# Optimization experiments

Measured on AMD Instinct MI355X. Metric: run time of the kernel, lower is better.

Reference implementation:

```python
import jax, jax.numpy as jnp
import numpy as np

B, T, C, H, NC = 512, 256, 512, 512, 96  # batch, encoder steps, channels, hidden, num classes


def setup_inputs() -> dict:
    key = jax.random.key(0)
    ks = jax.random.split(key, 12)
    def w(k, shape, fan):
        return (jax.random.normal(k, shape, jnp.float32) / np.sqrt(fan)).astype(jnp.float32)
    labels = jax.random.randint(ks[0], (B,), 0, NC)
    return {
        "prev_h": jax.random.normal(ks[1], (B, H), jnp.float32),
        "prev_c": jax.random.normal(ks[2], (B, H), jnp.float32),
        "batch_H": jax.random.normal(ks[3], (B, T, C), jnp.float32),
        "char_onehots": jax.nn.one_hot(labels, NC, dtype=jnp.float32),
        "Wi": w(ks[4], (C, H), C),            # i2h kernel (no bias)
        "Wh": w(ks[5], (H, H), H),            # h2h kernel
        "bh": jnp.zeros((H,), jnp.float32),    # h2h bias
        "Ws": w(ks[6], (H, 1), H),            # score kernel (no bias)
        "K": w(ks[7], (C + NC, 4 * H), C + NC),  # LSTM input kernel (i,f,g,o)
        "R": w(ks[8], (H, 4 * H), H),            # LSTM recurrent kernel
        "b": jnp.zeros((4 * H,), jnp.float32),    # LSTM bias
    }


def reference(prev_h, prev_c, batch_H, char_onehots, Wi, Wh, bh, Ws, K, R, b):
    # Additive (Bahdanau) attention
    proj = jnp.einsum('btc,ch->bth', batch_H, Wi)                  # [B,T,H]
    hp = prev_h @ Wh + bh                                          # [B,H]
    e = jnp.einsum('bth,h->bt', jnp.tanh(proj + hp[:, None, :]), Ws[:, 0])  # [B,T]
    alpha = jax.nn.softmax(e, axis=1)                              # [B,T]
    context = jnp.einsum('bt,btc->bc', alpha, batch_H)             # [B,C]
    # LSTMCell step (keras gate order: i, f, g, o; sigmoid recurrent act, tanh act)
    x = jnp.concatenate([context, char_onehots], axis=1)           # [B,C+NC]
    z = x @ K + prev_h @ R + b                                     # [B,4H]
    i, f, g, o = jnp.split(z, 4, axis=1)
    c_new = jax.nn.sigmoid(f) * prev_c + jax.nn.sigmoid(i) * jnp.tanh(g)
    h_new = jax.nn.sigmoid(o) * jnp.tanh(c_new)
    return (h_new, c_new, alpha[:, :, None])  # ((h,c), alpha[B,T,1])
```

## Files before the change

kernel.cpp:

```cpp
#include <hip/hip_runtime.h>
#include <hip/hip_bf16.h>
#include <stdint.h>

#define KFULL 1120
#define N4H   2048
#define MTOT  131072

typedef float f32x4 __attribute__((ext_vector_type(4)));
typedef __bf16 bf16x8 __attribute__((ext_vector_type(8)));
typedef unsigned short u16;

__device__ __forceinline__ u16 f2bf_bits(float f){
  __bf16 b = (__bf16)f;
  union { __bf16 b; u16 u; } cv; cv.b = b;
  return cv.u;
}
__device__ __forceinline__ float sigf(float x){ return 1.f / (1.f + __expf(-x)); }
__device__ __forceinline__ float tanh_fast(float x){ return 1.f - 2.f / (__expf(2.f * x) + 1.f); }
__device__ __forceinline__ int swz(int row){ return (row ^ (row >> 2)) & 3; }

__global__ void prep_w(const float* __restrict__ Wi, const float* __restrict__ Wh,
                       const float* __restrict__ Km, const float* __restrict__ R,
                       u16* __restrict__ wiT, u16* __restrict__ whT, u16* __restrict__ wfT){
  int idx = blockIdx.x * 256 + threadIdx.x;
  if (idx < 524288){
    const float* src = (idx < 262144) ? Wi : Wh;
    u16* dst = (idx < 262144) ? wiT : whT;
    int e = idx & 262143;
    int n = e & 511, kk = (e >> 9) & 31, s = e >> 14;
    float v = src[(size_t)(s * 32 + kk) * 512 + n];
    int dkk = (kk & 7) | ((((kk >> 3) ^ swz(n)) & 3) << 3);
    dst[((size_t)s * 512 + n) * 32 + dkk] = f2bf_bits(v);
  } else {
    int e = idx - 524288;
    if (e >= 35 * 2048 * 32) return;
    int n = e & 2047, kk = (e >> 11) & 31, s = e >> 16;
    int k = s * 32 + kk;
    float v = (k < 608) ? Km[(size_t)k * 2048 + n] : R[(size_t)(k - 608) * 2048 + n];
    int dkk = (kk & 7) | ((((kk >> 3) ^ swz(n)) & 3) << 3);
    wfT[((size_t)s * 2048 + n) * 32 + dkk] = f2bf_bits(v);
  }
}

__global__ void prep_x(const float* __restrict__ onehots, const float* __restrict__ prev_h,
                       float* __restrict__ x_full){
  int idx = blockIdx.x * 256 + threadIdx.x;
  if (idx >= 512 * 608) return;
  int b = idx / 608, c = idx % 608;
  float v = (c < 96) ? onehots[b * 96 + c] : prev_h[b * 512 + (c - 96)];
  x_full[(size_t)b * KFULL + 512 + c] = v;
}

template<int EPI>
__launch_bounds__(256, 3)
__global__ void gemm128(const float* __restrict__ A, int lda, int ksteps,
                        const u16* __restrict__ Bt, int ntot,
                        float* __restrict__ outp, size_t partStride,
                        const float* __restrict__ hpart, const float* __restrict__ bh,
                        const float* __restrict__ Ws, float* __restrict__ epart){
  __shared__ u16 smA[128 * 32];
  __shared__ u16 smB[128 * 32];
  __shared__ float smHp[128];
  __shared__ float smWs[128];
  __shared__ float smRed[2][128];

  const int tid  = threadIdx.x;
  const int lane = tid & 63, w = tid >> 6;
  const int wr = w >> 1, wc = w & 1;
  const int fr = lane & 15, g = lane >> 4;

  int m0, n0, s0;
  if (EPI == 1){
    int bid = blockIdx.x;
    int sw = (bid & 7) * 512 + (bid >> 3);
    m0 = (sw >> 2) * 128;
    n0 = (sw & 3) * 128;
    s0 = 0;
  } else {
    m0 = blockIdx.x * 128;
    n0 = blockIdx.y * 128;
    s0 = blockIdx.z * ksteps;
    outp += (size_t)blockIdx.z * partStride;
  }

  if (EPI == 1 && tid < 128){
    int b = m0 >> 8;
    float h = bh[n0 + tid];
    #pragma unroll
    for (int p = 0; p < 4; ++p) h += hpart[(size_t)p * 262144 + (size_t)b * 512 + n0 + tid];
    smHp[tid] = h;
    smWs[tid] = Ws[n0 + tid];
  }

  f32x4 acc[4][4] = {};

  const int ar = tid >> 2;
  const int ac = (tid & 3) * 8;
  const float* ap = A + (size_t)(m0 + ar) * lda + ac;
  const int sz  = swz(ar);
  const int ab0 = ar * 64 + (((tid & 3) ^ sz) << 4);
  const int ab1 = ab0 + 64 * 64;

  for (int s = 0; s < ksteps; ++s){
    const int kc = (s0 + s) * 32;
    const char* bsrc = (const char*)Bt + ((size_t)(s0 + s) * ntot + n0) * 64;
    #pragma unroll
    for (int j = 0; j < 2; ++j){
      int off = w * 2048 + j * 1024;
      __builtin_amdgcn_global_load_lds(
        (const __attribute__((address_space(1))) void*)(bsrc + off + lane * 16),
        (__attribute__((address_space(3))) void*)((char*)smB + off),
        16, 0, 0);
    }
    float4 a0 = *(const float4*)(ap + kc);
    float4 a1 = *(const float4*)(ap + kc + 4);
    float4 a2 = *(const float4*)(ap + (size_t)64 * lda + kc);
    float4 a3 = *(const float4*)(ap + (size_t)64 * lda + kc + 4);
    bf16x8 w0, w1;
    w0[0]=(__bf16)a0.x; w0[1]=(__bf16)a0.y; w0[2]=(__bf16)a0.z; w0[3]=(__bf16)a0.w;
    w0[4]=(__bf16)a1.x; w0[5]=(__bf16)a1.y; w0[6]=(__bf16)a1.z; w0[7]=(__bf16)a1.w;
    w1[0]=(__bf16)a2.x; w1[1]=(__bf16)a2.y; w1[2]=(__bf16)a2.z; w1[3]=(__bf16)a2.w;
    w1[4]=(__bf16)a3.x; w1[5]=(__bf16)a3.y; w1[6]=(__bf16)a3.z; w1[7]=(__bf16)a3.w;
    *(bf16x8*)((char*)smA + ab0) = w0;
    *(bf16x8*)((char*)smA + ab1) = w1;
    __syncthreads();

    bf16x8 af[4];
    #pragma unroll
    for (int m = 0; m < 4; ++m){
      int rl = wr * 64 + m * 16 + fr;
      af[m] = *(const bf16x8*)((const char*)smA + rl * 64 + ((g ^ swz(rl)) << 4));
    }
    #pragma unroll
    for (int n = 0; n < 4; ++n){
      int nl = wc * 64 + n * 16 + fr;
      bf16x8 bfv = *(const bf16x8*)((const char*)smB + nl * 64 + ((g ^ swz(nl)) << 4));
      #pragma unroll
      for (int m = 0; m < 4; ++m)
        acc[m][n] = __builtin_amdgcn_mfma_f32_16x16x32_bf16(af[m], bfv, acc[m][n], 0, 0, 0);
    }
    __syncthreads();
  }

  if (EPI == 0){
    #pragma unroll
    for (int n = 0; n < 4; ++n){
      int col = n0 + wc * 64 + n * 16 + fr;
      #pragma unroll
      for (int m = 0; m < 4; ++m){
        int row = m0 + wr * 64 + m * 16 + g * 4;
        #pragma unroll
        for (int j = 0; j < 4; ++j)
          outp[(size_t)(row + j) * ntot + col] = acc[m][n][j];
      }
    }
  } else {
    float p[16] = {};
    #pragma unroll
    for (int n = 0; n < 4; ++n){
      int col = wc * 64 + n * 16 + fr;
      float hpv = smHp[col], wsv = smWs[col];
      #pragma unroll
      for (int m = 0; m < 4; ++m)
        #pragma unroll
        for (int j = 0; j < 4; ++j)
          p[m * 4 + j] += tanh_fast(acc[m][n][j] + hpv) * wsv;
    }
    #pragma unroll
    for (int mask = 1; mask < 16; mask <<= 1)
      #pragma unroll
      for (int i = 0; i < 16; ++i)
        p[i] += __shfl_xor(p[i], mask);
    if (fr == 0){
      #pragma unroll
      for (int m = 0; m < 4; ++m)
        #pragma unroll
        for (int j = 0; j < 4; ++j)
          smRed[wc][wr * 64 + m * 16 + g * 4 + j] = p[m * 4 + j];
    }
    __syncthreads();
    if (tid < 128){
      int nb = n0 >> 7;
      epart[(size_t)nb * MTOT + m0 + tid] = smRed[0][tid] + smRed[1][tid];
    }
  }
}

__global__ void ctx_softmax(const float* __restrict__ epart, const float* __restrict__ batch_H,
                            float* __restrict__ x_full, float* __restrict__ alpha_out){
  __shared__ float sa[256];
  __shared__ float red[4], red2[4];
  __shared__ f32x4 sred[8][32];
  int b = blockIdx.x, q = blockIdx.y, tid = threadIdx.x;

  float e = 0.f;
  #pragma unroll
  for (int p = 0; p < 4; ++p) e += epart[(size_t)p * MTOT + b * 256 + tid];
  float m = e;
  #pragma unroll
  for (int mask = 1; mask < 64; mask <<= 1) m = fmaxf(m, __shfl_xor(m, mask));
  int w = tid >> 6;
  if ((tid & 63) == 0) red[w] = m;
  __syncthreads();
  m = fmaxf(fmaxf(red[0], red[1]), fmaxf(red[2], red[3]));
  float ev = __expf(e - m);
  float s = ev;
  #pragma unroll
  for (int mask = 1; mask < 64; mask <<= 1) s += __shfl_xor(s, mask);
  if ((tid & 63) == 0) red2[w] = s;
  __syncthreads();
  s = red2[0] + red2[1] + red2[2] + red2[3];
  float a = ev / s;
  sa[tid] = a;
  if (q == 0) alpha_out[(size_t)b * 256 + tid] = a;
  __syncthreads();

  int c4 = tid & 31, tq = tid >> 5;
  const float4* bhp = (const float4*)(batch_H + (size_t)b * 131072) + (size_t)tq * 32 * 128 + q * 32 + c4;
  f32x4 acc = {0.f, 0.f, 0.f, 0.f};
  #pragma unroll 4
  for (int t = 0; t < 32; ++t){
    float av = sa[tq * 32 + t];
    float4 v = bhp[(size_t)t * 128];
    acc[0] += av * v.x; acc[1] += av * v.y; acc[2] += av * v.z; acc[3] += av * v.w;
  }
  sred[tq][c4] = acc;
  __syncthreads();
  if (tid < 32){
    f32x4 o = sred[0][tid];
    #pragma unroll
    for (int r = 1; r < 8; ++r){
      f32x4 v = sred[r][tid];
      o[0] += v[0]; o[1] += v[1]; o[2] += v[2]; o[3] += v[3];
    }
    float4 st; st.x = o[0]; st.y = o[1]; st.z = o[2]; st.w = o[3];
    *(float4*)(x_full + (size_t)b * KFULL + q * 128 + tid * 4) = st;
  }
}

__global__ void gates_k(const float* __restrict__ zpart, const float* __restrict__ bias,
                        const float* __restrict__ prev_c, float* __restrict__ out){
  int idx = blockIdx.x * 256 + threadIdx.x;
  int b = idx >> 9, h = idx & 511;
  float zi = bias[h], zf = bias[512 + h], zg = bias[1024 + h], zo = bias[1536 + h];
  #pragma unroll
  for (int p = 0; p < 5; ++p){
    const float* zr = zpart + (size_t)p * 1048576 + (size_t)b * N4H;
    zi += zr[h]; zf += zr[512 + h]; zg += zr[1024 + h]; zo += zr[1536 + h];
  }
  float c = sigf(zf) * prev_c[idx] + sigf(zi) * tanh_fast(zg);
  float hn = sigf(zo) * tanh_fast(c);
  out[idx] = hn;
  out[262144 + idx] = c;
}

extern "C" void kernel_launch(void* const* d_in, const int* in_sizes, int n_in,
                              void* d_out, int out_size, void* d_ws, size_t ws_size,
                              hipStream_t stream){
  const float* prev_h  = (const float*)d_in[0];
  const float* prev_c  = (const float*)d_in[1];
  const float* batch_H = (const float*)d_in[2];
  const float* onehots = (const float*)d_in[3];
  const float* Wi      = (const float*)d_in[4];
  const float* Wh      = (const float*)d_in[5];
  const float* bh      = (const float*)d_in[6];
  const float* Ws      = (const float*)d_in[7];
  const float* Km      = (const float*)d_in[8];
  const float* R       = (const float*)d_in[9];
  const float* bb      = (const float*)d_in[10];
  float* out = (float*)d_out;

  char* ws = (char*)d_ws;
  u16*  wiT    = (u16*)(ws + 0);
  u16*  whT    = (u16*)(ws + 524288);
  u16*  wfT    = (u16*)(ws + 1048576);
  float* hpart = (float*)(ws + 5636096);
  float* epart = (float*)(ws + 9830400);
  float* x_full= (float*)(ws + 11927552);
  float* zpart = (float*)(ws + 14221312);

  float* alpha = out + 524288;

  prep_w<<<11008, 256, 0, stream>>>(Wi, Wh, Km, R, wiT, whT, wfT);
  prep_x<<<1216, 256, 0, stream>>>(onehots, prev_h, x_full);
  gemm128<0><<<dim3(4, 4, 4), 256, 0, stream>>>(prev_h, 512, 4, whT, 512,
                                                hpart, 262144, nullptr, nullptr, nullptr, nullptr);
  gemm128<1><<<dim3(4096, 1, 1), 256, 0, stream>>>(batch_H, 512, 16, wiT, 512,
                                                   nullptr, 0, hpart, bh, Ws, epart);
  ctx_softmax<<<dim3(512, 4), 256, 0, stream>>>(epart, batch_H, x_full, alpha);
  gemm128<0><<<dim3(4, 16, 5), 256, 0, stream>>>(x_full, KFULL, 7, wfT, N4H,
                                                 zpart, 1048576, nullptr, nullptr, nullptr, nullptr);
  gates_k<<<1024, 256, 0, stream>>>(zpart, bb, prev_c, out);
}
```

Before: 205.5 us.

## Split attention GEMM into double-buffered 512-thread kernel with 128x256 tiles

Replaces the templated attention GEMM with a dedicated kernel that uses 8 waves and 128x256 output tiles, so each A tile is loaded once per half of the hidden dimension instead of once per quarter. It double-buffers A and B in LDS and prefetches the next k-step with explicit waitcnt and barriers, overlapping global loads with MFMA work. The score partials drop from four to two per row, and the softmax kernel reads only two. The change costs more LDS and registers per block, which lowers occupancy, and relies on hand-placed waitcnt ordering being correct.

```diff
diff --git a/kernel.cpp b/kernel.cpp
--- a/kernel.cpp
+++ b/kernel.cpp
@@ -51,46 +51,21 @@
   x_full[(size_t)b * KFULL + 512 + c] = v;
 }
 
-template<int EPI>
 __launch_bounds__(256, 3)
-__global__ void gemm128(const float* __restrict__ A, int lda, int ksteps,
-                        const u16* __restrict__ Bt, int ntot,
-                        float* __restrict__ outp, size_t partStride,
-                        const float* __restrict__ hpart, const float* __restrict__ bh,
-                        const float* __restrict__ Ws, float* __restrict__ epart){
+__global__ void gemm_small(const float* __restrict__ A, int lda, int ksteps,
+                           const u16* __restrict__ Bt, int ntot,
+                           float* __restrict__ outp, size_t partStride){
   __shared__ u16 smA[128 * 32];
   __shared__ u16 smB[128 * 32];
-  __shared__ float smHp[128];
-  __shared__ float smWs[128];
-  __shared__ float smRed[2][128];
 
   const int tid  = threadIdx.x;
   const int lane = tid & 63, w = tid >> 6;
   const int wr = w >> 1, wc = w & 1;
   const int fr = lane & 15, g = lane >> 4;
-
-  int m0, n0, s0;
-  if (EPI == 1){
-    int bid = blockIdx.x;
-    int sw = (bid & 7) * 512 + (bid >> 3);
-    m0 = (sw >> 2) * 128;
-    n0 = (sw & 3) * 128;
-    s0 = 0;
-  } else {
-    m0 = blockIdx.x * 128;
-    n0 = blockIdx.y * 128;
-    s0 = blockIdx.z * ksteps;
-    outp += (size_t)blockIdx.z * partStride;
-  }
-
-  if (EPI == 1 && tid < 128){
-    int b = m0 >> 8;
-    float h = bh[n0 + tid];
-    #pragma unroll
-    for (int p = 0; p < 4; ++p) h += hpart[(size_t)p * 262144 + (size_t)b * 512 + n0 + tid];
-    smHp[tid] = h;
-    smWs[tid] = Ws[n0 + tid];
-  }
+  const int m0 = blockIdx.x * 128;
+  const int n0 = blockIdx.y * 128;
+  const int s0 = blockIdx.z * ksteps;
+  outp += (size_t)blockIdx.z * partStride;
 
   f32x4 acc[4][4] = {};
 
@@ -142,48 +117,154 @@
     __syncthreads();
   }
 
-  if (EPI == 0){
-    #pragma unroll
-    for (int n = 0; n < 4; ++n){
-      int col = n0 + wc * 64 + n * 16 + fr;
+  #pragma unroll
+  for (int n = 0; n < 4; ++n){
+    int col = n0 + wc * 64 + n * 16 + fr;
+    #pragma unroll
+    for (int m = 0; m < 4; ++m){
+      int row = m0 + wr * 64 + m * 16 + g * 4;
       #pragma unroll
-      for (int m = 0; m < 4; ++m){
-        int row = m0 + wr * 64 + m * 16 + g * 4;
-        #pragma unroll
-        for (int j = 0; j < 4; ++j)
-          outp[(size_t)(row + j) * ntot + col] = acc[m][n][j];
-      }
-    }
-  } else {
-    float p[16] = {};
-    #pragma unroll
-    for (int n = 0; n < 4; ++n){
-      int col = wc * 64 + n * 16 + fr;
-      float hpv = smHp[col], wsv = smWs[col];
+      for (int j = 0; j < 4; ++j)
+        outp[(size_t)(row + j) * ntot + col] = acc[m][n][j];
+    }
+  }
+}
+
+__launch_bounds__(512, 2)
+__global__ void gemm_attn(const float* __restrict__ A,
+                          const u16* __restrict__ Bt,
+                          const float* __restrict__ hpart,
+                          const float* __restrict__ bh,
+                          const float* __restrict__ Wsv,
+                          float* __restrict__ epart){
+  __shared__ u16 smA[2][128 * 32];
+  __shared__ u16 smB[2][256 * 32];
+  __shared__ float smHp[256];
+  __shared__ float smWs[256];
+  __shared__ float smRed[4][128];
+
+  const int tid  = threadIdx.x;
+  const int lane = tid & 63, w = tid >> 6;
+  const int wr = w >> 2, wc = w & 3;
+  const int fr = lane & 15, g = lane >> 4;
+  const int m0 = blockIdx.x * 128;
+  const int nb = blockIdx.y;
+  const int n0 = nb * 256;
+  const int b  = blockIdx.x >> 1;
+
+  if (tid < 256){
+    float h = bh[n0 + tid];
+    #pragma unroll
+    for (int p = 0; p < 4; ++p) h += hpart[(size_t)p * 262144 + (size_t)b * 512 + n0 + tid];
+    smHp[tid] = h;
+    smWs[tid] = Wsv[n0 + tid];
+  }
+  asm volatile("s_waitcnt vmcnt(0) lgkmcnt(0)" ::: "memory");
+
+  f32x4 acc[4][4] = {};
+
+  const int arow = tid >> 2;
+  const int achk = tid & 3;
+  const float* aglob = A + (size_t)(m0 + arow) * 512 + achk * 8;
+  const int awoff = arow * 64 + ((achk ^ swz(arow)) << 4);
+
+  float4 pa0, pa1;
+
+#define ISSUE_B(sabs, c) do {                                              \
+    const char* bsrc = (const char*)Bt + ((size_t)(sabs) * 512 + n0) * 64; \
+    _Pragma("unroll")                                                      \
+    for (int j = 0; j < 2; ++j){                                           \
+      int off = j * 8192 + w * 1024;                                       \
+      __builtin_amdgcn_global_load_lds(                                    \
+        (const __attribute__((address_space(1))) void*)(bsrc + off + lane * 16), \
+        (__attribute__((address_space(3))) void*)((char*)&smB[c][0] + off),\
+        16, 0, 0);                                                         \
+    }                                                                      \
+  } while(0)
+
+#define LOAD_A(sabs) do {                                                  \
+    pa0 = *(const float4*)(aglob + (size_t)(sabs) * 32);                   \
+    pa1 = *(const float4*)(aglob + (size_t)(sabs) * 32 + 4);               \
+  } while(0)
+
+#define WRITE_A(c) do {                                                    \
+    bf16x8 v;                                                              \
+    v[0]=(__bf16)pa0.x; v[1]=(__bf16)pa0.y; v[2]=(__bf16)pa0.z; v[3]=(__bf16)pa0.w; \
+    v[4]=(__bf16)pa1.x; v[5]=(__bf16)pa1.y; v[6]=(__bf16)pa1.z; v[7]=(__bf16)pa1.w; \
+    *(bf16x8*)((char*)&smA[c][0] + awoff) = v;                             \
+  } while(0)
+
+#define COMPUTE(c) do {                                                    \
+    bf16x8 af[4];                                                          \
+    _Pragma("unroll")                                                      \
+    for (int m = 0; m < 4; ++m){                                           \
+      int rl = wr * 64 + m * 16 + fr;                                      \
+      af[m] = *(const bf16x8*)((const char*)&smA[c][0] + rl * 64 + ((g ^ swz(rl)) << 4)); \
+    }                                                                      \
+    _Pragma("unroll")                                                      \
+    for (int n = 0; n < 4; ++n){                                           \
+      int nl = wc * 64 + n * 16 + fr;                                      \
+      bf16x8 bfv = *(const bf16x8*)((const char*)&smB[c][0] + nl * 64 + ((g ^ swz(nl)) << 4)); \
+      _Pragma("unroll")                                                    \
+      for (int m = 0; m < 4; ++m)                                          \
+        acc[m][n] = __builtin_amdgcn_mfma_f32_16x16x32_bf16(af[m], bfv, acc[m][n], 0, 0, 0); \
+    }                                                                      \
+  } while(0)
+
+  LOAD_A(0);
+  ISSUE_B(0, 0);
+  asm volatile("" ::: "memory");
+  WRITE_A(0);
+  LOAD_A(1);
+
+  for (int s = 0; s < 16; ++s){
+    if (s < 15) asm volatile("s_waitcnt vmcnt(2)" ::: "memory");
+    else        asm volatile("s_waitcnt vmcnt(0)" ::: "memory");
+    asm volatile("s_waitcnt lgkmcnt(0)" ::: "memory");
+    __builtin_amdgcn_s_barrier();
+    asm volatile("" ::: "memory");
+    COMPUTE(s & 1);
+    if (s < 15){
+      ISSUE_B(s + 1, (s + 1) & 1);
+      asm volatile("" ::: "memory");
+      WRITE_A((s + 1) & 1);
+      if (s < 14) LOAD_A(s + 2);
+    }
+  }
+
+#undef ISSUE_B
+#undef LOAD_A
+#undef WRITE_A
+#undef COMPUTE
+
+  float p[16] = {};
+  #pragma unroll
+  for (int n = 0; n < 4; ++n){
+    int col = wc * 64 + n * 16 + fr;
+    float hpv = smHp[col], wsv = smWs[col];
+    #pragma unroll
+    for (int m = 0; m < 4; ++m)
       #pragma unroll
-      for (int m = 0; m < 4; ++m)
-        #pragma unroll
-        for (int j = 0; j < 4; ++j)
-          p[m * 4 + j] += tanh_fast(acc[m][n][j] + hpv) * wsv;
-    }
-    #pragma unroll
-    for (int mask = 1; mask < 16; mask <<= 1)
+      for (int j = 0; j < 4; ++j)
+        p[m * 4 + j] += tanh_fast(acc[m][n][j] + hpv) * wsv;
+  }
+  #pragma unroll
+  for (int mask = 1; mask < 16; mask <<= 1)
+    #pragma unroll
+    for (int i = 0; i < 16; ++i)
+      p[i] += __shfl_xor(p[i], mask);
+  __syncthreads();
+  if (fr == 0){
+    #pragma unroll
+    for (int m = 0; m < 4; ++m)
       #pragma unroll
-      for (int i = 0; i < 16; ++i)
-        p[i] += __shfl_xor(p[i], mask);
-    if (fr == 0){
-      #pragma unroll
-      for (int m = 0; m < 4; ++m)
-        #pragma unroll
-        for (int j = 0; j < 4; ++j)
-          smRed[wc][wr * 64 + m * 16 + g * 4 + j] = p[m * 4 + j];
-    }
-    __syncthreads();
-    if (tid < 128){
-      int nb = n0 >> 7;
-      epart[(size_t)nb * MTOT + m0 + tid] = smRed[0][tid] + smRed[1][tid];
-    }
-  }
+      for (int j = 0; j < 4; ++j)
+        smRed[wc][wr * 64 + m * 16 + g * 4 + j] = p[m * 4 + j];
+  }
+  __syncthreads();
+  if (tid < 128)
+    epart[(size_t)nb * MTOT + m0 + tid] =
+      smRed[0][tid] + smRed[1][tid] + smRed[2][tid] + smRed[3][tid];
 }
 
 __global__ void ctx_softmax(const float* __restrict__ epart, const float* __restrict__ batch_H,
@@ -193,9 +274,7 @@
   __shared__ f32x4 sred[8][32];
   int b = blockIdx.x, q = blockIdx.y, tid = threadIdx.x;
 
-  float e = 0.f;
-  #pragma unroll
-  for (int p = 0; p < 4; ++p) e += epart[(size_t)p * MTOT + b * 256 + tid];
+  float e = epart[(size_t)b * 256 + tid] + epart[MTOT + (size_t)b * 256 + tid];
   float m = e;
   #pragma unroll
   for (int mask = 1; mask < 64; mask <<= 1) m = fmaxf(m, __shfl_xor(m, mask));
@@ -283,12 +362,11 @@
 
   prep_w<<<11008, 256, 0, stream>>>(Wi, Wh, Km, R, wiT, whT, wfT);
   prep_x<<<1216, 256, 0, stream>>>(onehots, prev_h, x_full);
-  gemm128<0><<<dim3(4, 4, 4), 256, 0, stream>>>(prev_h, 512, 4, whT, 512,
-                                                hpart, 262144, nullptr, nullptr, nullptr, nullptr);
-  gemm128<1><<<dim3(4096, 1, 1), 256, 0, stream>>>(batch_H, 512, 16, wiT, 512,
-                                                   nullptr, 0, hpart, bh, Ws, epart);
+  gemm_small<<<dim3(4, 4, 4), 256, 0, stream>>>(prev_h, 512, 4, whT, 512,
+                                                hpart, 262144);
+  gemm_attn<<<dim3(1024, 2), 512, 0, stream>>>(batch_H, wiT, hpart, bh, Ws, epart);
   ctx_softmax<<<dim3(512, 4), 256, 0, stream>>>(epart, batch_H, x_full, alpha);
-  gemm128<0><<<dim3(4, 16, 5), 256, 0, stream>>>(x_full, KFULL, 7, wfT, N4H,
-                                                 zpart, 1048576, nullptr, nullptr, nullptr, nullptr);
+  gemm_small<<<dim3(4, 16, 5), 256, 0, stream>>>(x_full, KFULL, 7, wfT, N4H,
+                                                 zpart, 1048576);
   gates_k<<<1024, 256, 0, stream>>>(zpart, bb, prev_c, out);
 }
```

After: 209.2 us. About the same (+1.8%).

## Restructure attention GEMM: whole-K A tile in LDS, B fragments from global

Applied to the files above, without the earlier changes.

The fused attention-score GEMM now uses 64x256 tiles: each block loads its full 64-row A slab (all 16 K-steps) into LDS once as bf16 and streams Wi fragments straight from global into registers with double buffering, dropping the per-step syncthreads. Wi is stored unswizzled so per-lane global reads are contiguous. The N split shrinks from 4 to 2 partials, so softmax sums two partials. This removes per-K-step barriers and LDS staging for B, at the cost of 64KB LDS per block, more registers and lower occupancy (launch bounds 2).

```diff
diff --git a/kernel.cpp b/kernel.cpp
--- a/kernel.cpp
+++ b/kernel.cpp
@@ -29,7 +29,8 @@
     int e = idx & 262143;
     int n = e & 511, kk = (e >> 9) & 31, s = e >> 14;
     float v = src[(size_t)(s * 32 + kk) * 512 + n];
-    int dkk = (kk & 7) | ((((kk >> 3) ^ swz(n)) & 3) << 3);
+    int dkk = (idx < 262144) ? kk
+            : ((kk & 7) | ((((kk >> 3) ^ swz(n)) & 3) << 3));
     dst[((size_t)s * 512 + n) * 32 + dkk] = f2bf_bits(v);
   } else {
     int e = idx - 524288;
@@ -51,46 +52,21 @@
   x_full[(size_t)b * KFULL + 512 + c] = v;
 }
 
-template<int EPI>
 __launch_bounds__(256, 3)
-__global__ void gemm128(const float* __restrict__ A, int lda, int ksteps,
-                        const u16* __restrict__ Bt, int ntot,
-                        float* __restrict__ outp, size_t partStride,
-                        const float* __restrict__ hpart, const float* __restrict__ bh,
-                        const float* __restrict__ Ws, float* __restrict__ epart){
+__global__ void gemm_small(const float* __restrict__ A, int lda, int ksteps,
+                           const u16* __restrict__ Bt, int ntot,
+                           float* __restrict__ outp, size_t partStride){
   __shared__ u16 smA[128 * 32];
   __shared__ u16 smB[128 * 32];
-  __shared__ float smHp[128];
-  __shared__ float smWs[128];
-  __shared__ float smRed[2][128];
 
   const int tid  = threadIdx.x;
   const int lane = tid & 63, w = tid >> 6;
   const int wr = w >> 1, wc = w & 1;
   const int fr = lane & 15, g = lane >> 4;
-
-  int m0, n0, s0;
-  if (EPI == 1){
-    int bid = blockIdx.x;
-    int sw = (bid & 7) * 512 + (bid >> 3);
-    m0 = (sw >> 2) * 128;
-    n0 = (sw & 3) * 128;
-    s0 = 0;
-  } else {
-    m0 = blockIdx.x * 128;
-    n0 = blockIdx.y * 128;
-    s0 = blockIdx.z * ksteps;
-    outp += (size_t)blockIdx.z * partStride;
-  }
-
-  if (EPI == 1 && tid < 128){
-    int b = m0 >> 8;
-    float h = bh[n0 + tid];
-    #pragma unroll
-    for (int p = 0; p < 4; ++p) h += hpart[(size_t)p * 262144 + (size_t)b * 512 + n0 + tid];
-    smHp[tid] = h;
-    smWs[tid] = Ws[n0 + tid];
-  }
+  const int m0 = blockIdx.x * 128;
+  const int n0 = blockIdx.y * 128;
+  const int s0 = blockIdx.z * ksteps;
+  outp += (size_t)blockIdx.z * partStride;
 
   f32x4 acc[4][4] = {};
 
@@ -142,48 +118,133 @@
     __syncthreads();
   }
 
-  if (EPI == 0){
+  #pragma unroll
+  for (int n = 0; n < 4; ++n){
+    int col = n0 + wc * 64 + n * 16 + fr;
+    #pragma unroll
+    for (int m = 0; m < 4; ++m){
+      int row = m0 + wr * 64 + m * 16 + g * 4;
+      #pragma unroll
+      for (int j = 0; j < 4; ++j)
+        outp[(size_t)(row + j) * ntot + col] = acc[m][n][j];
+    }
+  }
+}
+
+__launch_bounds__(256, 2)
+__global__ void gemm_attn(const float* __restrict__ A,
+                          const u16* __restrict__ Bt,
+                          const float* __restrict__ hpart,
+                          const float* __restrict__ bh,
+                          const float* __restrict__ Wsv,
+                          float* __restrict__ epart){
+  __shared__ u16 smA[16][64 * 32];
+
+  const int tid  = threadIdx.x;
+  const int lane = tid & 63, w = tid >> 6;
+  const int fr = lane & 15, g = lane >> 4;
+  const int bid = blockIdx.x;
+  const int m0 = (bid >> 1) * 64;
+  const int nb = bid & 1;
+  const int n0 = nb * 256;
+  const int b  = m0 >> 8;
+
+  const int arow = tid >> 2;
+  const float* ag = A + (size_t)(m0 + arow) * 512 + (tid & 3) * 8;
+  const int awbase = arow * 64 + (((tid & 3) ^ swz(arow)) << 4);
+  float4 av[32];
+  #pragma unroll
+  for (int s = 0; s < 16; ++s){
+    av[2 * s]     = *(const float4*)(ag + s * 32);
+    av[2 * s + 1] = *(const float4*)(ag + s * 32 + 4);
+  }
+  #pragma unroll
+  for (int s = 0; s < 16; ++s){
+    bf16x8 v;
+    v[0]=(__bf16)av[2*s].x;   v[1]=(__bf16)av[2*s].y;
+    v[2]=(__bf16)av[2*s].z;   v[3]=(__bf16)av[2*s].w;
+    v[4]=(__bf16)av[2*s+1].x; v[5]=(__bf16)av[2*s+1].y;
+    v[6]=(__bf16)av[2*s+1].z; v[7]=(__bf16)av[2*s+1].w;
+    *(bf16x8*)((char*)&smA[s][0] + awbase) = v;
+  }
+
+  float hpv[4], wsv[4];
+  #pragma unroll
+  for (int n = 0; n < 4; ++n){
+    int col = n0 + w * 64 + n * 16 + fr;
+    float h = bh[col];
+    #pragma unroll
+    for (int p = 0; p < 4; ++p) h += hpart[(size_t)p * 262144 + (size_t)b * 512 + col];
+    hpv[n] = h;
+    wsv[n] = Wsv[col];
+  }
+
+  __syncthreads();
+
+  const u16* bbase = Bt + ((size_t)(n0 + w * 64 + fr)) * 32 + g * 8;
+  bf16x8 bA[4], bB[4];
+  #pragma unroll
+  for (int nf = 0; nf < 4; ++nf)
+    bA[nf] = *(const bf16x8*)(bbase + (size_t)nf * 16 * 32);
+
+  f32x4 acc[4][4] = {};
+
+  #pragma unroll
+  for (int s = 0; s < 16; ++s){
+    if (s + 1 < 16){
+      if ((s & 1) == 0){
+        #pragma unroll
+        for (int nf = 0; nf < 4; ++nf)
+          bB[nf] = *(const bf16x8*)(bbase + ((size_t)(s + 1) * 512 + nf * 16) * 32);
+      } else {
+        #pragma unroll
+        for (int nf = 0; nf < 4; ++nf)
+          bA[nf] = *(const bf16x8*)(bbase + ((size_t)(s + 1) * 512 + nf * 16) * 32);
+      }
+    }
+    bf16x8 af[4];
+    #pragma unroll
+    for (int m = 0; m < 4; ++m){
+      int rl = m * 16 + fr;
+      af[m] = *(const bf16x8*)((const char*)&smA[s][0] + rl * 64 + ((g ^ swz(rl)) << 4));
+    }
     #pragma unroll
     for (int n = 0; n < 4; ++n){
-      int col = n0 + wc * 64 + n * 16 + fr;
-      #pragma unroll
-      for (int m = 0; m < 4; ++m){
-        int row = m0 + wr * 64 + m * 16 + g * 4;
-        #pragma unroll
-        for (int j = 0; j < 4; ++j)
-          outp[(size_t)(row + j) * ntot + col] = acc[m][n][j];
-      }
-    }
-  } else {
-    float p[16] = {};
-    #pragma unroll
-    for (int n = 0; n < 4; ++n){
-      int col = wc * 64 + n * 16 + fr;
-      float hpv = smHp[col], wsv = smWs[col];
+      bf16x8 bfv = ((s & 1) == 0) ? bA[n] : bB[n];
       #pragma unroll
       for (int m = 0; m < 4; ++m)
-        #pragma unroll
-        for (int j = 0; j < 4; ++j)
-          p[m * 4 + j] += tanh_fast(acc[m][n][j] + hpv) * wsv;
-    }
-    #pragma unroll
-    for (int mask = 1; mask < 16; mask <<= 1)
-      #pragma unroll
-      for (int i = 0; i < 16; ++i)
-        p[i] += __shfl_xor(p[i], mask);
-    if (fr == 0){
-      #pragma unroll
-      for (int m = 0; m < 4; ++m)
-        #pragma unroll
-        for (int j = 0; j < 4; ++j)
-          smRed[wc][wr * 64 + m * 16 + g * 4 + j] = p[m * 4 + j];
-    }
-    __syncthreads();
-    if (tid < 128){
-      int nb = n0 >> 7;
-      epart[(size_t)nb * MTOT + m0 + tid] = smRed[0][tid] + smRed[1][tid];
-    }
-  }
+        acc[m][n] = __builtin_amdgcn_mfma_f32_16x16x32_bf16(af[m], bfv, acc[m][n], 0, 0, 0);
+    }
+  }
+
+  float p[16] = {};
+  #pragma unroll
+  for (int n = 0; n < 4; ++n){
+    #pragma unroll
+    for (int m = 0; m < 4; ++m)
+      #pragma unroll
+      for (int j = 0; j < 4; ++j)
+        p[m * 4 + j] += tanh_fast(acc[m][n][j] + hpv[n]) * wsv[n];
+  }
+  #pragma unroll
+  for (int mask = 1; mask < 16; mask <<= 1)
+    #pragma unroll
+    for (int i = 0; i < 16; ++i)
+      p[i] += __shfl_xor(p[i], mask);
+
+  float* smRed = (float*)&smA[0][0];
+  __syncthreads();
+  if (fr == 0){
+    #pragma unroll
+    for (int m = 0; m < 4; ++m)
+      #pragma unroll
+      for (int j = 0; j < 4; ++j)
+        smRed[w * 64 + m * 16 + g * 4 + j] = p[m * 4 + j];
+  }
+  __syncthreads();
+  if (tid < 64)
+    epart[(size_t)nb * MTOT + m0 + tid] =
+      smRed[tid] + smRed[64 + tid] + smRed[128 + tid] + smRed[192 + tid];
 }
 
 __global__ void ctx_softmax(const float* __restrict__ epart, const float* __restrict__ batch_H,
@@ -193,9 +254,7 @@
   __shared__ f32x4 sred[8][32];
   int b = blockIdx.x, q = blockIdx.y, tid = threadIdx.x;
 
-  float e = 0.f;
-  #pragma unroll
-  for (int p = 0; p < 4; ++p) e += epart[(size_t)p * MTOT + b * 256 + tid];
+  float e = epart[(size_t)b * 256 + tid] + epart[MTOT + (size_t)b * 256 + tid];
   float m = e;
   #pragma unroll
   for (int mask = 1; mask < 64; mask <<= 1) m = fmaxf(m, __shfl_xor(m, mask));
@@ -283,12 +342,11 @@
 
   prep_w<<<11008, 256, 0, stream>>>(Wi, Wh, Km, R, wiT, whT, wfT);
   prep_x<<<1216, 256, 0, stream>>>(onehots, prev_h, x_full);
-  gemm128<0><<<dim3(4, 4, 4), 256, 0, stream>>>(prev_h, 512, 4, whT, 512,
-                                                hpart, 262144, nullptr, nullptr, nullptr, nullptr);
-  gemm128<1><<<dim3(4096, 1, 1), 256, 0, stream>>>(batch_H, 512, 16, wiT, 512,
-                                                   nullptr, 0, hpart, bh, Ws, epart);
+  gemm_small<<<dim3(4, 4, 4), 256, 0, stream>>>(prev_h, 512, 4, whT, 512,
+                                                hpart, 262144);
+  gemm_attn<<<4096, 256, 0, stream>>>(batch_H, wiT, hpart, bh, Ws, epart);
   ctx_softmax<<<dim3(512, 4), 256, 0, stream>>>(epart, batch_H, x_full, alpha);
-  gemm128<0><<<dim3(4, 16, 5), 256, 0, stream>>>(x_full, KFULL, 7, wfT, N4H,
-                                                 zpart, 1048576, nullptr, nullptr, nullptr, nullptr);
+  gemm_small<<<dim3(4, 16, 5), 256, 0, stream>>>(x_full, KFULL, 7, wfT, N4H,
+                                                 zpart, 1048576);
   gates_k<<<1024, 256, 0, stream>>>(zpart, bb, prev_c, out);
 }
```

Measured after the change: 245.4 us. 19.4% more time.
